# Performance work log

Hardware: AMD Instinct MI355X
Metric: run time of the kernel (lower is better)

## Reference

```python
import jax, jax.numpy as jnp
import numpy as np

N_NODES = 50000
N_EDGES = 800000
IN_DIM = 128
OUT_DIM = 64


def setup_inputs() -> dict:
    key = jax.random.key(0)
    k1, k2, k3, k4, k5 = jax.random.split(key, 5)
    x = jax.random.normal(k1, (N_NODES, IN_DIM), dtype=jnp.float32)
    # Glorot-uniform-ish init for the GCN weight (weight_variable_glorot)
    limit = np.sqrt(6.0 / (IN_DIM + OUT_DIM)).astype(np.float32)
    weight = jax.random.uniform(k2, (IN_DIM, OUT_DIM), dtype=jnp.float32,
                                minval=-limit, maxval=limit)
    adj_row = jax.random.randint(k3, (N_EDGES,), 0, N_NODES, dtype=jnp.int32)
    adj_col = jax.random.randint(k4, (N_EDGES,), 0, N_NODES, dtype=jnp.int32)
    adj_val = jax.random.uniform(k5, (N_EDGES,), dtype=jnp.float32)
    return {"x": x, "weight": weight, "adj_row": adj_row,
            "adj_col": adj_col, "adj_val": adj_val}


def reference(x, weight, adj_row, adj_col, adj_val):
    # x: [N, F_in], weight: [F_in, F_out]; dropout=0.0 (default) is identity.
    xw = jnp.matmul(x, weight)                      # [N, F_out] dense GEMM
    # spmm(adj, xw) with adj in COO: gather neighbor feats, scale, scatter-add
    msg = adj_val[:, None] * xw[adj_col]            # [E, F_out]
    agg = jax.ops.segment_sum(msg, adj_row, num_segments=x.shape[0])  # [N, F_out]
    return jax.nn.relu(agg)
```

## Files before the change

### kernel.cpp

```cpp
#include <hip/hip_runtime.h>

#define IN_DIM 128
#define OUT_DIM 64
#define PADK 136
#define RB 64
#define RBSH 6
#define CAPB 1280
#define AB2 256

typedef float f32x4 __attribute__((ext_vector_type(4)));
typedef short bf16x8 __attribute__((ext_vector_type(8)));

__device__ __forceinline__ unsigned short f2bf(float f) {
    unsigned u = __float_as_uint(f);
    return (unsigned short)((u + 0x7FFFu + ((u >> 16) & 1u)) >> 16);
}
__device__ __forceinline__ float bf2f(unsigned short h) {
    return __uint_as_float((unsigned)h << 16);
}

__device__ __forceinline__ void gemm_body(const float* __restrict__ x,
                                          const float* __restrict__ w,
                                          unsigned short* __restrict__ xwb,
                                          int N, int blk,
                                          unsigned short* lds) {
    unsigned short* Bhi = lds;
    unsigned short* Blo = lds + 64 * PADK;

    const int t = threadIdx.x;
    const int r0 = blk * 64;

    {
        const int c = t >> 2;
        const int kb = (t & 3) * 32;
        for (int k4 = 0; k4 < 32; k4 += 4) {
            ushort4 h, l;
            float v0 = w[(kb + k4 + 0) * OUT_DIM + c];
            float v1 = w[(kb + k4 + 1) * OUT_DIM + c];
            float v2 = w[(kb + k4 + 2) * OUT_DIM + c];
            float v3 = w[(kb + k4 + 3) * OUT_DIM + c];
            h.x = f2bf(v0); l.x = f2bf(v0 - bf2f(h.x));
            h.y = f2bf(v1); l.y = f2bf(v1 - bf2f(h.y));
            h.z = f2bf(v2); l.z = f2bf(v2 - bf2f(h.z));
            h.w = f2bf(v3); l.w = f2bf(v3 - bf2f(h.w));
            *(ushort4*)&Bhi[c * PADK + kb + k4] = h;
            *(ushort4*)&Blo[c * PADK + kb + k4] = l;
        }
    }

    const int lane = t & 63;
    const int wv = t >> 6;
    const int m = lane & 15;
    const int quad = lane >> 4;

    int row = r0 + wv * 16 + m; if (row >= N) row = N - 1;
    const float4* xr = (const float4*)(x + (size_t)row * IN_DIM);
    bf16x8 ahi[4], alo[4];
#pragma unroll
    for (int ks = 0; ks < 4; ++ks) {
        const float4 v0 = xr[ks * 8 + quad * 2];
        const float4 v1 = xr[ks * 8 + quad * 2 + 1];
        float f[8] = {v0.x, v0.y, v0.z, v0.w, v1.x, v1.y, v1.z, v1.w};
        bf16x8 h8, l8;
#pragma unroll
        for (int i = 0; i < 8; ++i) {
            const unsigned short h = f2bf(f[i]);
            h8[i] = (short)h;
            l8[i] = (short)f2bf(f[i] - bf2f(h));
        }
        ahi[ks] = h8; alo[ks] = l8;
    }
    __syncthreads();

#pragma unroll
    for (int ct = 0; ct < 4; ++ct) {
        f32x4 acc = {0.f, 0.f, 0.f, 0.f};
#pragma unroll
        for (int ks = 0; ks < 4; ++ks) {
            const int off = (ct * 16 + m) * PADK + ks * 32 + quad * 8;
            bf16x8 bh = *(const bf16x8*)&Bhi[off];
            bf16x8 bl = *(const bf16x8*)&Blo[off];
            acc = __builtin_amdgcn_mfma_f32_16x16x32_bf16(alo[ks], bh, acc, 0, 0, 0);
            acc = __builtin_amdgcn_mfma_f32_16x16x32_bf16(ahi[ks], bl, acc, 0, 0, 0);
            acc = __builtin_amdgcn_mfma_f32_16x16x32_bf16(ahi[ks], bh, acc, 0, 0, 0);
        }
#pragma unroll
        for (int i = 0; i < 4; ++i) {
            const int r = r0 + wv * 16 + quad * 4 + i;
            if (r < N) xwb[(size_t)r * OUT_DIM + ct * 16 + m] = f2bf(acc[i]);
        }
    }
}

__device__ __forceinline__ void afill_body(
        const int* __restrict__ arow, const int* __restrict__ acol,
        const float* __restrict__ aval, int* __restrict__ pcur,
        int* __restrict__ ocount, uint4* __restrict__ olist,
        uint2* __restrict__ payload, int E, int NB, int chunk, int blk,
        int* ldsi) {
    int* cnt  = ldsi;
    int* base = ldsi + 1024;
    const int t = threadIdx.x;
    const int lo = blk * chunk;
    const int hi = min(E, lo + chunk);
    if (lo >= hi) return;
    const int len = hi - lo;
    const int n4  = len >> 2;
    const int4*   ar4 = (const int4*)(arow + lo);
    const int4*   ac4 = (const int4*)(acol + lo);
    const float4* av4 = (const float4*)(aval + lo);

    for (int i = t; i < NB; i += 256) cnt[i] = 0;
    __syncthreads();

    for (int j = t; j < n4; j += 256) {
        const int4 r = ar4[j];
        atomicAdd(&cnt[r.x >> RBSH], 1);
        atomicAdd(&cnt[r.y >> RBSH], 1);
        atomicAdd(&cnt[r.z >> RBSH], 1);
        atomicAdd(&cnt[r.w >> RBSH], 1);
    }
    for (int e = lo + (n4 << 2) + t; e < hi; e += 256)
        atomicAdd(&cnt[arow[e] >> RBSH], 1);
    __syncthreads();

    for (int i = t; i < NB; i += 256) {
        const int c = cnt[i];
        base[i] = c ? atomicAdd(&pcur[i], c) : 0;
        cnt[i] = 0;
    }
    __syncthreads();

#define AF_EMIT(RR, CC, VV) do {                                              \
        const int b_ = (RR) >> RBSH;                                          \
        const int slot_ = base[b_] + atomicAdd(&cnt[b_], 1);                  \
        const unsigned w0_ = (unsigned)(CC) |                                 \
                             ((unsigned)((RR) & (RB - 1)) << 16);             \
        const unsigned w1_ = __float_as_uint(VV);                             \
        if (slot_ < CAPB) {                                                   \
            payload[(size_t)b_ * CAPB + slot_] = make_uint2(w0_, w1_);        \
        } else {                                                              \
            const int oi_ = atomicAdd(ocount, 1);                             \
            olist[oi_] = make_uint4((unsigned)(RR), (unsigned)(CC), w1_, 0u); \
        }                                                                     \
    } while (0)

    for (int j = t; j < n4; j += 256) {
        const int4   r = ar4[j];
        const int4   c = ac4[j];
        const float4 v = av4[j];
        AF_EMIT(r.x, c.x, v.x);
        AF_EMIT(r.y, c.y, v.y);
        AF_EMIT(r.z, c.z, v.z);
        AF_EMIT(r.w, c.w, v.w);
    }
    for (int e = lo + (n4 << 2) + t; e < hi; e += 256)
        AF_EMIT(arow[e], acol[e], aval[e]);
#undef AF_EMIT
}

__global__ __launch_bounds__(256) void gemm_afill(
        const float* __restrict__ x, const float* __restrict__ w,
        unsigned short* __restrict__ xwb, int N,
        const int* __restrict__ arow, const int* __restrict__ acol,
        const float* __restrict__ aval, int* __restrict__ pcur,
        int* __restrict__ ocount, uint4* __restrict__ olist,
        uint2* __restrict__ payload, int E, int NB, int chunk) {
    __shared__ unsigned short LB[2 * 64 * PADK];
    if ((int)blockIdx.x < AB2) {
        afill_body(arow, acol, aval, pcur, ocount, olist, payload, E, NB,
                   chunk, blockIdx.x, (int*)LB);
    } else {
        gemm_body(x, w, xwb, N, blockIdx.x - AB2, LB);
    }
}

__global__ __launch_bounds__(256) void gemm_only(const float* __restrict__ x,
                                                 const float* __restrict__ w,
                                                 unsigned short* __restrict__ xwb,
                                                 int N) {
    __shared__ unsigned short LB[2 * 64 * PADK];
    gemm_body(x, w, xwb, N, blockIdx.x, LB);
}

__global__ __launch_bounds__(512) void bagg3(
        const int* __restrict__ pcur, const uint2* __restrict__ payload,
        const unsigned short* __restrict__ xwb, float* __restrict__ out, int N,
        const int* __restrict__ ocount, const uint4* __restrict__ olist) {
    __shared__ uint2 stage[CAPB];
    __shared__ int bins[RB + 1];
    __shared__ int pl[RB];
    const int t = threadIdx.x;
    const int lane = t & 63;
    const int wv = t >> 6;
    const int b = blockIdx.x;
    const int r0 = b << RBSH;

    const int cnt = min(pcur[b], CAPB);
    if (t <= RB) bins[t] = 0;
    if (t < RB) pl[t] = 0;
    __syncthreads();

    const uint2* pay = payload + (size_t)b * CAPB;
    for (int i = t; i < cnt; i += 512)
        atomicAdd(&bins[(pay[i].x >> 16) & (RB - 1)], 1);
    __syncthreads();
    if (t < RB) {
        const int v = bins[t];
        int s = v;
#pragma unroll
        for (int d = 1; d < RB; d <<= 1) {
            const int u = __shfl_up(s, d, 64);
            if (t >= d) s += u;
        }
        bins[t + 1] = s;
        if (t == 0) bins[0] = 0;
    }
    __syncthreads();
    for (int i = t; i < cnt; i += 512) {
        const uint2 e = pay[i];
        const int rl = (e.x >> 16) & (RB - 1);
        stage[bins[rl] + atomicAdd(&pl[rl], 1)] = e;
    }
    __syncthreads();

    float acc[8];
#pragma unroll
    for (int lr = 0; lr < 8; ++lr) {
        const int row = wv * 8 + lr;
        int j = bins[row];
        const int end = bins[row + 1];
        float a0 = 0.f, a1 = 0.f;
        for (; j + 8 <= end; j += 8) {
            uint2 e0 = stage[j],   e1 = stage[j+1], e2 = stage[j+2], e3 = stage[j+3];
            uint2 e4 = stage[j+4], e5 = stage[j+5], e6 = stage[j+6], e7 = stage[j+7];
            float g0 = bf2f(xwb[(size_t)(e0.x & 0xFFFF) * OUT_DIM + lane]);
            float g1 = bf2f(xwb[(size_t)(e1.x & 0xFFFF) * OUT_DIM + lane]);
            float g2 = bf2f(xwb[(size_t)(e2.x & 0xFFFF) * OUT_DIM + lane]);
            float g3 = bf2f(xwb[(size_t)(e3.x & 0xFFFF) * OUT_DIM + lane]);
            float g4 = bf2f(xwb[(size_t)(e4.x & 0xFFFF) * OUT_DIM + lane]);
            float g5 = bf2f(xwb[(size_t)(e5.x & 0xFFFF) * OUT_DIM + lane]);
            float g6 = bf2f(xwb[(size_t)(e6.x & 0xFFFF) * OUT_DIM + lane]);
            float g7 = bf2f(xwb[(size_t)(e7.x & 0xFFFF) * OUT_DIM + lane]);
            a0 = fmaf(__uint_as_float(e0.y), g0, a0);
            a1 = fmaf(__uint_as_float(e1.y), g1, a1);
            a0 = fmaf(__uint_as_float(e2.y), g2, a0);
            a1 = fmaf(__uint_as_float(e3.y), g3, a1);
            a0 = fmaf(__uint_as_float(e4.y), g4, a0);
            a1 = fmaf(__uint_as_float(e5.y), g5, a1);
            a0 = fmaf(__uint_as_float(e6.y), g6, a0);
            a1 = fmaf(__uint_as_float(e7.y), g7, a1);
        }
        for (; j + 4 <= end; j += 4) {
            uint2 e0 = stage[j], e1 = stage[j+1], e2 = stage[j+2], e3 = stage[j+3];
            float g0 = bf2f(xwb[(size_t)(e0.x & 0xFFFF) * OUT_DIM + lane]);
            float g1 = bf2f(xwb[(size_t)(e1.x & 0xFFFF) * OUT_DIM + lane]);
            float g2 = bf2f(xwb[(size_t)(e2.x & 0xFFFF) * OUT_DIM + lane]);
            float g3 = bf2f(xwb[(size_t)(e3.x & 0xFFFF) * OUT_DIM + lane]);
            a0 = fmaf(__uint_as_float(e0.y), g0, a0);
            a1 = fmaf(__uint_as_float(e1.y), g1, a1);
            a0 = fmaf(__uint_as_float(e2.y), g2, a0);
            a1 = fmaf(__uint_as_float(e3.y), g3, a1);
        }
        for (; j < end; ++j) {
            uint2 e0 = stage[j];
            a0 = fmaf(__uint_as_float(e0.y),
                      bf2f(xwb[(size_t)(e0.x & 0xFFFF) * OUT_DIM + lane]), a0);
        }
        acc[lr] = a0 + a1;
    }

    const int oc = *ocount;
    for (int i = 0; i < oc; ++i) {
        const uint4 e = olist[i];
        const int lr = (int)e.x - r0 - wv * 8;
        if (lr >= 0 && lr < 8)
            acc[lr] += __uint_as_float(e.z) *
                       bf2f(xwb[(size_t)e.y * OUT_DIM + lane]);
    }

#pragma unroll
    for (int lr = 0; lr < 8; ++lr) {
        const int row = r0 + wv * 8 + lr;
        if (row < N) {
            const float v = acc[lr];
            out[(size_t)row * OUT_DIM + lane] = v > 0.f ? v : 0.f;
        }
    }
}

__global__ __launch_bounds__(256) void scatter_edges(
        const int* __restrict__ arow, const int* __restrict__ acol,
        const float* __restrict__ aval, const unsigned short* __restrict__ xwb,
        float* __restrict__ out, int E) {
    const int lane = threadIdx.x & 63;
    int gw = (blockIdx.x * 256 + (int)threadIdx.x) >> 6;
    const int nw = (gridDim.x * 256) >> 6;
    for (int e = gw; e < E; e += nw) {
        const float m = aval[e] * bf2f(xwb[(size_t)acol[e] * OUT_DIM + lane]);
        atomicAdd(&out[(size_t)arow[e] * OUT_DIM + lane], m);
    }
}

__global__ __launch_bounds__(256) void relu_inplace(float* __restrict__ o, int n4) {
    float4* p = (float4*)o;
    int i = blockIdx.x * 256 + threadIdx.x;
    const int stride = gridDim.x * 256;
    for (; i < n4; i += stride) {
        float4 v = p[i];
        v.x = v.x > 0.f ? v.x : 0.f;
        v.y = v.y > 0.f ? v.y : 0.f;
        v.z = v.z > 0.f ? v.z : 0.f;
        v.w = v.w > 0.f ? v.w : 0.f;
        p[i] = v;
    }
}

static inline size_t align256(size_t x) { return (x + 255) & ~(size_t)255; }

extern "C" void kernel_launch(void* const* d_in, const int* in_sizes, int n_in,
                              void* d_out, int out_size, void* d_ws, size_t ws_size,
                              hipStream_t stream) {
    const float* x    = (const float*)d_in[0];
    const float* w    = (const float*)d_in[1];
    const int*   arow = (const int*)d_in[2];
    const int*   acol = (const int*)d_in[3];
    const float* aval = (const float*)d_in[4];
    float*       out  = (float*)d_out;

    const int N  = in_sizes[0] / IN_DIM;
    const int E  = in_sizes[2];
    const int NB = (N + RB - 1) >> RBSH;
    const int GB = (N + 63) / 64;

    char* ws = (char*)d_ws;
    const size_t szXW  = align256((size_t)N * OUT_DIM * sizeof(unsigned short));
    const size_t szCnt = align256((size_t)(NB + 1) * sizeof(int));
    const size_t szOl  = align256((size_t)E * sizeof(uint4));
    const size_t szPay = (size_t)NB * CAPB * sizeof(uint2);
    const size_t need0 = szXW + szCnt + szOl + szPay;

    unsigned short* xwb = (unsigned short*)ws;
    int*   pcur    = (int*)(ws + szXW);
    int*   ocount  = pcur + NB;
    uint4* olist   = (uint4*)(ws + szXW + szCnt);
    uint2* payload = (uint2*)(ws + szXW + szCnt + szOl);

    if (ws_size >= need0 && N <= 65536 && NB <= 1024) {
        (void)hipMemsetAsync(pcur, 0, (size_t)(NB + 1) * sizeof(int), stream);
        const int chunk = (((E + AB2 - 1) / AB2) + 3) & ~3;
        gemm_afill<<<AB2 + GB, 256, 0, stream>>>(x, w, xwb, N, arow, acol, aval,
                                                 pcur, ocount, olist, payload,
                                                 E, NB, chunk);
        bagg3<<<NB, 512, 0, stream>>>(pcur, payload, xwb, out, N, ocount, olist);
    } else {
        gemm_only<<<GB, 256, 0, stream>>>(x, w, xwb, N);
        (void)hipMemsetAsync(d_out, 0, (size_t)out_size * sizeof(float), stream);
        scatter_edges<<<4096, 256, 0, stream>>>(arow, acol, aval, xwb, out, E);
        relu_inplace<<<2048, 256, 0, stream>>>(out, out_size / 4);
    }
}
```

Baseline: 125.5 us.

## Replace per-row LDS counting sort with LDS float-atomic accumulation tile

The aggregation kernel no longer bins each block's edges by local row with a histogram, scan and scatter into a sorted stage buffer. Instead it copies the edge payload into LDS as-is, distributes edges across waves in groups of eight, and accumulates messages with LDS float atomics into a 64x64 output tile. The tile is then ReLU'd and written with coalesced float4 stores. This removes three barriers and the sort passes, at the cost of an LDS atomic per edge per lane, a larger LDS footprint (16KB tile plus the edge buffer), and nondeterministic summation order.

```diff
diff --git a/kernel.cpp b/kernel.cpp
--- a/kernel.cpp
+++ b/kernel.cpp
@@ -17,6 +17,14 @@
 }
 __device__ __forceinline__ float bf2f(unsigned short h) {
     return __uint_as_float((unsigned)h << 16);
+}
+
+__device__ __forceinline__ void lds_fadd(float* p, float v) {
+#if defined(__HIP_PLATFORM_AMD__) || defined(__AMDGCN__)
+    unsafeAtomicAdd(p, v);
+#else
+    atomicAdd(p, v);
+#endif
 }
 
 __device__ __forceinline__ void gemm_body(const float* __restrict__ x,
@@ -183,13 +191,12 @@
     gemm_body(x, w, xwb, N, blockIdx.x, LB);
 }
 
-__global__ __launch_bounds__(512) void bagg3(
+__global__ __launch_bounds__(512) void bagg5(
         const int* __restrict__ pcur, const uint2* __restrict__ payload,
         const unsigned short* __restrict__ xwb, float* __restrict__ out, int N,
         const int* __restrict__ ocount, const uint4* __restrict__ olist) {
-    __shared__ uint2 stage[CAPB];
-    __shared__ int bins[RB + 1];
-    __shared__ int pl[RB];
+    __shared__ float otile[RB * OUT_DIM];
+    __shared__ uint2 eb[CAPB];
     const int t = threadIdx.x;
     const int lane = t & 63;
     const int wv = t >> 6;
@@ -197,43 +204,18 @@
     const int r0 = b << RBSH;
 
     const int cnt = min(pcur[b], CAPB);
-    if (t <= RB) bins[t] = 0;
-    if (t < RB) pl[t] = 0;
-    __syncthreads();
-
+
+#pragma unroll
+    for (int i = t; i < RB * OUT_DIM; i += 512) otile[i] = 0.f;
     const uint2* pay = payload + (size_t)b * CAPB;
-    for (int i = t; i < cnt; i += 512)
-        atomicAdd(&bins[(pay[i].x >> 16) & (RB - 1)], 1);
-    __syncthreads();
-    if (t < RB) {
-        const int v = bins[t];
-        int s = v;
-#pragma unroll
-        for (int d = 1; d < RB; d <<= 1) {
-            const int u = __shfl_up(s, d, 64);
-            if (t >= d) s += u;
-        }
-        bins[t + 1] = s;
-        if (t == 0) bins[0] = 0;
-    }
-    __syncthreads();
-    for (int i = t; i < cnt; i += 512) {
-        const uint2 e = pay[i];
-        const int rl = (e.x >> 16) & (RB - 1);
-        stage[bins[rl] + atomicAdd(&pl[rl], 1)] = e;
-    }
-    __syncthreads();
-
-    float acc[8];
-#pragma unroll
-    for (int lr = 0; lr < 8; ++lr) {
-        const int row = wv * 8 + lr;
-        int j = bins[row];
-        const int end = bins[row + 1];
-        float a0 = 0.f, a1 = 0.f;
-        for (; j + 8 <= end; j += 8) {
-            uint2 e0 = stage[j],   e1 = stage[j+1], e2 = stage[j+2], e3 = stage[j+3];
-            uint2 e4 = stage[j+4], e5 = stage[j+5], e6 = stage[j+6], e7 = stage[j+7];
+    for (int i = t; i < cnt; i += 512) eb[i] = pay[i];
+    __syncthreads();
+
+    for (int base = wv * 8; base < cnt; base += 64) {
+        const int m = min(8, cnt - base);
+        if (m == 8) {
+            uint2 e0 = eb[base+0], e1 = eb[base+1], e2 = eb[base+2], e3 = eb[base+3];
+            uint2 e4 = eb[base+4], e5 = eb[base+5], e6 = eb[base+6], e7 = eb[base+7];
             float g0 = bf2f(xwb[(size_t)(e0.x & 0xFFFF) * OUT_DIM + lane]);
             float g1 = bf2f(xwb[(size_t)(e1.x & 0xFFFF) * OUT_DIM + lane]);
             float g2 = bf2f(xwb[(size_t)(e2.x & 0xFFFF) * OUT_DIM + lane]);
@@ -242,50 +224,46 @@
             float g5 = bf2f(xwb[(size_t)(e5.x & 0xFFFF) * OUT_DIM + lane]);
             float g6 = bf2f(xwb[(size_t)(e6.x & 0xFFFF) * OUT_DIM + lane]);
             float g7 = bf2f(xwb[(size_t)(e7.x & 0xFFFF) * OUT_DIM + lane]);
-            a0 = fmaf(__uint_as_float(e0.y), g0, a0);
-            a1 = fmaf(__uint_as_float(e1.y), g1, a1);
-            a0 = fmaf(__uint_as_float(e2.y), g2, a0);
-            a1 = fmaf(__uint_as_float(e3.y), g3, a1);
-            a0 = fmaf(__uint_as_float(e4.y), g4, a0);
-            a1 = fmaf(__uint_as_float(e5.y), g5, a1);
-            a0 = fmaf(__uint_as_float(e6.y), g6, a0);
-            a1 = fmaf(__uint_as_float(e7.y), g7, a1);
-        }
-        for (; j + 4 <= end; j += 4) {
-            uint2 e0 = stage[j], e1 = stage[j+1], e2 = stage[j+2], e3 = stage[j+3];
-            float g0 = bf2f(xwb[(size_t)(e0.x & 0xFFFF) * OUT_DIM + lane]);
-            float g1 = bf2f(xwb[(size_t)(e1.x & 0xFFFF) * OUT_DIM + lane]);
-            float g2 = bf2f(xwb[(size_t)(e2.x & 0xFFFF) * OUT_DIM + lane]);
-            float g3 = bf2f(xwb[(size_t)(e3.x & 0xFFFF) * OUT_DIM + lane]);
-            a0 = fmaf(__uint_as_float(e0.y), g0, a0);
-            a1 = fmaf(__uint_as_float(e1.y), g1, a1);
-            a0 = fmaf(__uint_as_float(e2.y), g2, a0);
-            a1 = fmaf(__uint_as_float(e3.y), g3, a1);
-        }
-        for (; j < end; ++j) {
-            uint2 e0 = stage[j];
-            a0 = fmaf(__uint_as_float(e0.y),
-                      bf2f(xwb[(size_t)(e0.x & 0xFFFF) * OUT_DIM + lane]), a0);
-        }
-        acc[lr] = a0 + a1;
+            lds_fadd(&otile[((e0.x >> 16) & 63) * OUT_DIM + lane], __uint_as_float(e0.y) * g0);
+            lds_fadd(&otile[((e1.x >> 16) & 63) * OUT_DIM + lane], __uint_as_float(e1.y) * g1);
+            lds_fadd(&otile[((e2.x >> 16) & 63) * OUT_DIM + lane], __uint_as_float(e2.y) * g2);
+            lds_fadd(&otile[((e3.x >> 16) & 63) * OUT_DIM + lane], __uint_as_float(e3.y) * g3);
+            lds_fadd(&otile[((e4.x >> 16) & 63) * OUT_DIM + lane], __uint_as_float(e4.y) * g4);
+            lds_fadd(&otile[((e5.x >> 16) & 63) * OUT_DIM + lane], __uint_as_float(e5.y) * g5);
+            lds_fadd(&otile[((e6.x >> 16) & 63) * OUT_DIM + lane], __uint_as_float(e6.y) * g6);
+            lds_fadd(&otile[((e7.x >> 16) & 63) * OUT_DIM + lane], __uint_as_float(e7.y) * g7);
+        } else {
+            for (int k = 0; k < m; ++k) {
+                const uint2 e0 = eb[base + k];
+                const float g0 = bf2f(xwb[(size_t)(e0.x & 0xFFFF) * OUT_DIM + lane]);
+                lds_fadd(&otile[((e0.x >> 16) & 63) * OUT_DIM + lane],
+                         __uint_as_float(e0.y) * g0);
+            }
+        }
     }
 
     const int oc = *ocount;
     for (int i = 0; i < oc; ++i) {
         const uint4 e = olist[i];
-        const int lr = (int)e.x - r0 - wv * 8;
-        if (lr >= 0 && lr < 8)
-            acc[lr] += __uint_as_float(e.z) *
-                       bf2f(xwb[(size_t)e.y * OUT_DIM + lane]);
-    }
-
-#pragma unroll
-    for (int lr = 0; lr < 8; ++lr) {
-        const int row = r0 + wv * 8 + lr;
-        if (row < N) {
-            const float v = acc[lr];
-            out[(size_t)row * OUT_DIM + lane] = v > 0.f ? v : 0.f;
-        }
+        const int rl = (int)e.x - r0;
+        if (rl >= 0 && rl < RB && wv == (i & 7)) {
+            const float g = bf2f(xwb[(size_t)e.y * OUT_DIM + lane]);
+            lds_fadd(&otile[rl * OUT_DIM + lane], __uint_as_float(e.z) * g);
+        }
+    }
+    __syncthreads();
+
+    const int nvalid = min(RB, N - r0);
+    const int n4 = nvalid * (OUT_DIM / 4);
+    const float4* ot4 = (const float4*)otile;
+    float4* o4 = (float4*)(out + (size_t)r0 * OUT_DIM);
+    for (int i = t; i < n4; i += 512) {
+        float4 v = ot4[i];
+        v.x = v.x > 0.f ? v.x : 0.f;
+        v.y = v.y > 0.f ? v.y : 0.f;
+        v.z = v.z > 0.f ? v.z : 0.f;
+        v.w = v.w > 0.f ? v.w : 0.f;
+        o4[i] = v;
     }
 }
 
@@ -352,7 +330,7 @@
         gemm_afill<<<AB2 + GB, 256, 0, stream>>>(x, w, xwb, N, arow, acol, aval,
                                                  pcur, ocount, olist, payload,
                                                  E, NB, chunk);
-        bagg3<<<NB, 512, 0, stream>>>(pcur, payload, xwb, out, N, ocount, olist);
+        bagg5<<<NB, 512, 0, stream>>>(pcur, payload, xwb, out, N, ocount, olist);
     } else {
         gemm_only<<<GB, 256, 0, stream>>>(x, w, xwb, N);
         (void)hipMemsetAsync(d_out, 0, (size_t)out_size * sizeof(float), stream);
```

Result: slower. 444.5 us (+254.3%).
